# Kernel tuning notes

Hardware: AMD Instinct MI355X
Metric: run time of the kernel (lower is better)

Reference implementation:

```python
import jax, jax.numpy as jnp
import numpy as np

USER_NUM = 100000
ITEM_NUM = 100000  # padding index; table has ITEM_NUM+1 rows
D = 64
B = 4096
L = 200
NEG_WEIGHT = 0.1


def setup_inputs() -> dict:
    key = jax.random.key(0)
    k1, k2, k3, k4, k5 = jax.random.split(key, 5)
    uids = jax.random.randint(k1, (B,), 0, USER_NUM, dtype=jnp.int64 if jax.config.jax_enable_x64 else jnp.int32)
    pos_iids = jax.random.randint(k2, (B, L), 0, ITEM_NUM + 1, dtype=jnp.int64 if jax.config.jax_enable_x64 else jnp.int32)
    user_W = jax.random.normal(k3, (USER_NUM, D), dtype=jnp.float32) * 0.1
    item_W = jax.random.normal(k4, (ITEM_NUM + 1, D), dtype=jnp.float32) * 0.1
    h = jnp.full((D, 1), 0.01, dtype=jnp.float32)  # reset_para: constant 0.01
    return {"uids": uids, "pos_iids": pos_iids, "user_W": user_W, "item_W": item_W, "h": h}


def reference(uids, pos_iids, user_W, item_W, h):
    u_emb = user_W[uids]                      # [B, D] (dropout p=0 -> identity)
    pos_embs = item_W[pos_iids]               # [B, L, D]
    mask = (pos_iids != ITEM_NUM).astype(u_emb.dtype)  # padding id masked out
    pos_embs = pos_embs * mask[:, :, None]
    # hpq[b,l] = sum_d u[b,d] * pos[b,l,d] * h[d]
    hpq = jnp.einsum('bd,bld,d->bl', u_emb, pos_embs, h[:, 0])
    pos_data_loss = jnp.sum((1.0 - NEG_WEIGHT) * jnp.square(hpq) - 2.0 * hpq)
    # part_1/part_2 in torch are sums of per-row outer products == Gram matrices
    part_1 = item_W.T @ item_W                # [D, D]
    part_2 = u_emb.T @ u_emb                  # [D, D]
    part_3 = h @ h.T                          # [D, D]
    all_data_loss = jnp.sum(part_1 * part_2 * part_3)
    return NEG_WEIGHT * all_data_loss + pos_data_loss
```

## Files before the change

### kernel.cpp

```cpp
#include <hip/hip_runtime.h>

#define D 64
#define ITEM_PAD 100000
#define LSEQ 200
#define BATCH 4096
#define NEG_W 0.1f
#define NBI 512
#define NBU 64
#define GSZ (D * D)
#define PITEM_OFF 0
#define PUSER_OFF ((size_t)NBI * GSZ)
#define POS_OFF   (PUSER_OFF + (size_t)NBU * GSZ)
#define WS2_OFF   (POS_OFF + BATCH)
#define CTR_OFF   (WS2_OFF + 256)

__global__ void fused_partials(const int* __restrict__ uids,
                               const int* __restrict__ pos_iids,
                               const float* __restrict__ user_W,
                               const float* __restrict__ item_W,
                               const float* __restrict__ h,
                               float* __restrict__ ws) {
    __shared__ float smem[32 * D];
    const int bid = blockIdx.x;
    const int t   = threadIdx.x;

    if (bid == 0 && t == 0) ((unsigned*)(ws + CTR_OFF))[0] = 0u;

    if (bid < NBI + NBU) {
        const bool item = (bid < NBI);
        const float* __restrict__ W = item ? item_W : user_W;
        const int* __restrict__ idx = item ? nullptr : uids;
        const int nrows  = item ? (ITEM_PAD + 1) : BATCH;
        const int stride = item ? NBI : NBU;
        const int b0     = item ? bid : bid - NBI;
        float* __restrict__ out =
            ws + (item ? PITEM_OFF + (size_t)b0 * GSZ : PUSER_OFF + (size_t)b0 * GSZ);

        const int ti = t >> 4;
        const int tj = t & 15;
        float acc[4][4] = {{0.f,0.f,0.f,0.f},{0.f,0.f,0.f,0.f},
                           {0.f,0.f,0.f,0.f},{0.f,0.f,0.f,0.f}};

        const int nchunks = (nrows + 31) >> 5;

        float4 va = make_float4(0.f,0.f,0.f,0.f), vb = va;
        int c = b0;
        if (c < nchunks) {
            const int ra = (c << 5) + ti, rb = ra + 16;
            if (ra < nrows) {
                const int sa = idx ? idx[ra] : ra;
                va = *(const float4*)(W + (size_t)sa * D + tj * 4);
            }
            if (rb < nrows) {
                const int sb = idx ? idx[rb] : rb;
                vb = *(const float4*)(W + (size_t)sb * D + tj * 4);
            }
        }

        for (; c < nchunks; ) {
            __syncthreads();
            *(float4*)(smem + ti * D + tj * 4)        = va;
            *(float4*)(smem + (ti + 16) * D + tj * 4) = vb;
            __syncthreads();

            const int cn = c + stride;
            va = make_float4(0.f,0.f,0.f,0.f); vb = va;
            if (cn < nchunks) {
                const int ra = (cn << 5) + ti, rb = ra + 16;
                if (ra < nrows) {
                    const int sa = idx ? idx[ra] : ra;
                    va = *(const float4*)(W + (size_t)sa * D + tj * 4);
                }
                if (rb < nrows) {
                    const int sb = idx ? idx[rb] : rb;
                    vb = *(const float4*)(W + (size_t)sb * D + tj * 4);
                }
            }

            #pragma unroll
            for (int r2 = 0; r2 < 32; ++r2) {
                float xi[4], xj[4];
                *(float4*)xi = *(const float4*)(smem + r2 * D + ti * 4);
                *(float4*)xj = *(const float4*)(smem + r2 * D + tj * 4);
                #pragma unroll
                for (int a = 0; a < 4; ++a)
                    #pragma unroll
                    for (int b2 = 0; b2 < 4; ++b2)
                        acc[a][b2] += xi[a] * xj[b2];
            }
            c = cn;
        }
        #pragma unroll
        for (int a = 0; a < 4; ++a)
            *(float4*)(out + (ti * 4 + a) * D + tj * 4) = *(const float4*)acc[a];
    } else {
        const int b = bid - (NBI + NBU);
        float* uh   = smem;
        int*   sidx = (int*)(smem + D);
        float* red  = smem + D + LSEQ;

        if (t < LSEQ) sidx[t] = pos_iids[(size_t)b * LSEQ + t];
        if (t >= 192) {
            const int j = t - 192;
            uh[j] = user_W[(size_t)uids[b] * D + j] * h[j];
        }
        __syncthreads();

        const int lane = t & 63;
        const int wave = t >> 6;
        const int p    = lane >> 4;
        const int q    = lane & 15;
        const int base = wave * 4 + p;

        const float4 u4 = *(const float4*)(uh + q * 4);

        int ids[13];
        #pragma unroll
        for (int k = 0; k < 13; ++k) {
            const int l = base + 16 * k;
            ids[k] = (l < LSEQ) ? sidx[l] : ITEM_PAD;
        }
        float4 rows[13];
        #pragma unroll
        for (int k = 0; k < 13; ++k) {
            float4 v = make_float4(0.f, 0.f, 0.f, 0.f);
            if (ids[k] != ITEM_PAD)
                v = *(const float4*)(item_W + (size_t)ids[k] * D + q * 4);
            rows[k] = v;
        }

        float local = 0.f;
        #pragma unroll
        for (int k = 0; k < 13; ++k) {
            float s = u4.x*rows[k].x + u4.y*rows[k].y + u4.z*rows[k].z + u4.w*rows[k].w;
            s += __shfl_xor(s, 1);
            s += __shfl_xor(s, 2);
            s += __shfl_xor(s, 4);
            s += __shfl_xor(s, 8);
            if (q == 0)
                local += (1.0f - NEG_W) * s * s - 2.0f * s;
        }
        local += __shfl_xor(local, 1);
        local += __shfl_xor(local, 2);
        local += __shfl_xor(local, 4);
        local += __shfl_xor(local, 8);
        local += __shfl_xor(local, 16);
        local += __shfl_xor(local, 32);
        if (lane == 0) red[wave] = local;
        __syncthreads();
        if (t == 0)
            ws[POS_OFF + b] = red[0] + red[1] + red[2] + red[3];
    }
}

__global__ void reduce_final(const float* __restrict__ ws,
                             const float* __restrict__ h,
                             float* __restrict__ ws2,
                             unsigned* __restrict__ counter,
                             float* __restrict__ out) {
    __shared__ float rI[4][16];
    __shared__ float rU[4][16];
    __shared__ int isLast;
    const int b  = blockIdx.x;
    const int t  = threadIdx.x;
    const int kk = t & 15;
    const int ps = t >> 4;
    const int lane = t & 63;
    const int wave = t >> 6;
    const int k  = b * 16 + kk;

    float si = 0.f, su = 0.f;
    #pragma unroll 8
    for (int p = ps; p < NBI; p += 16) si += ws[PITEM_OFF + (size_t)p * GSZ + k];
    #pragma unroll
    for (int p = ps; p < NBU; p += 16) su += ws[PUSER_OFF + (size_t)p * GSZ + k];

    si += __shfl_xor(si, 16); si += __shfl_xor(si, 32);
    su += __shfl_xor(su, 16); su += __shfl_xor(su, 32);
    if (lane < 16) { rI[wave][kk] = si; rU[wave][kk] = su; }
    __syncthreads();

    float c = 0.f;
    if (t < 16) {
        const float Gi = rI[0][t] + rI[1][t] + rI[2][t] + rI[3][t];
        const float Gu = rU[0][t] + rU[1][t] + rU[2][t] + rU[3][t];
        const int kg = b * 16 + t;
        const int i = kg >> 6, j = kg & 63;
        c = NEG_W * Gi * Gu * h[i] * h[j] + ws[POS_OFF + b * 16 + t];
    }
    if (wave == 0) {
        c += __shfl_xor(c, 1);
        c += __shfl_xor(c, 2);
        c += __shfl_xor(c, 4);
        c += __shfl_xor(c, 8);
        if (lane == 0) ws2[b] = c;
    }

    if (t == 0) {
        __threadfence();
        const unsigned old = atomicAdd(counter, 1u);
        isLast = (old == 255u);
    }
    __syncthreads();
    if (isLast) {
        __threadfence();
        float s = ws2[t];
        s += __shfl_xor(s, 1);
        s += __shfl_xor(s, 2);
        s += __shfl_xor(s, 4);
        s += __shfl_xor(s, 8);
        s += __shfl_xor(s, 16);
        s += __shfl_xor(s, 32);
        __shared__ float red[4];
        if (lane == 0) red[wave] = s;
        __syncthreads();
        if (t == 0) out[0] = red[0] + red[1] + red[2] + red[3];
    }
}

extern "C" void kernel_launch(void* const* d_in, const int* in_sizes, int n_in,
                              void* d_out, int out_size, void* d_ws, size_t ws_size,
                              hipStream_t stream) {
    const int*   uids     = (const int*)d_in[0];
    const int*   pos_iids = (const int*)d_in[1];
    const float* user_W   = (const float*)d_in[2];
    const float* item_W   = (const float*)d_in[3];
    const float* h        = (const float*)d_in[4];
    float* out = (float*)d_out;
    float* ws  = (float*)d_ws;

    fused_partials<<<NBI + NBU + BATCH, 256, 0, stream>>>(uids, pos_iids, user_W,
                                                          item_W, h, ws);
    reduce_final<<<256, 256, 0, stream>>>(ws, h, ws + WS2_OFF,
                                          (unsigned*)(ws + CTR_OFF), out);
}
```

Before: 130.8 us.

## Convert item table to bf16 during Gram pass and gather bf16 rows for scores

```diff
diff --git a/kernel.cpp b/kernel.cpp
--- a/kernel.cpp
+++ b/kernel.cpp
@@ -8,45 +8,87 @@
 #define NBI 512
 #define NBU 64
 #define GSZ (D * D)
-#define PITEM_OFF 0
-#define PUSER_OFF ((size_t)NBI * GSZ)
-#define POS_OFF   (PUSER_OFF + (size_t)NBU * GSZ)
-#define WS2_OFF   (POS_OFF + BATCH)
-#define CTR_OFF   (WS2_OFF + 256)
-
-__global__ void fused_partials(const int* __restrict__ uids,
-                               const int* __restrict__ pos_iids,
-                               const float* __restrict__ user_W,
-                               const float* __restrict__ item_W,
-                               const float* __restrict__ h,
-                               float* __restrict__ ws) {
+
+#define BFT_FLOATS 3200032
+#define PITEM_OFF  ((size_t)BFT_FLOATS)
+#define PUSER_OFF  (PITEM_OFF + (size_t)NBI * GSZ)
+#define POS_OFF    (PUSER_OFF + (size_t)NBU * GSZ)
+#define GDOT_OFF   (POS_OFF + BATCH)
+
+__device__ __forceinline__ unsigned short f2bf_rne(float x) {
+    unsigned u = __builtin_bit_cast(unsigned, x);
+    return (unsigned short)((u + 0x7fffu + ((u >> 16) & 1u)) >> 16);
+}
+__device__ __forceinline__ float bf_lo(unsigned u) {
+    return __builtin_bit_cast(float, u << 16);
+}
+__device__ __forceinline__ float bf_hi(unsigned u) {
+    return __builtin_bit_cast(float, u & 0xffff0000u);
+}
+
+__global__ void gram_convert(const int* __restrict__ uids,
+                             const float* __restrict__ user_W,
+                             const float* __restrict__ item_W,
+                             float* __restrict__ ws) {
     __shared__ float smem[32 * D];
     const int bid = blockIdx.x;
     const int t   = threadIdx.x;
 
-    if (bid == 0 && t == 0) ((unsigned*)(ws + CTR_OFF))[0] = 0u;
-
-    if (bid < NBI + NBU) {
-        const bool item = (bid < NBI);
-        const float* __restrict__ W = item ? item_W : user_W;
-        const int* __restrict__ idx = item ? nullptr : uids;
-        const int nrows  = item ? (ITEM_PAD + 1) : BATCH;
-        const int stride = item ? NBI : NBU;
-        const int b0     = item ? bid : bid - NBI;
-        float* __restrict__ out =
-            ws + (item ? PITEM_OFF + (size_t)b0 * GSZ : PUSER_OFF + (size_t)b0 * GSZ);
-
-        const int ti = t >> 4;
-        const int tj = t & 15;
-        float acc[4][4] = {{0.f,0.f,0.f,0.f},{0.f,0.f,0.f,0.f},
-                           {0.f,0.f,0.f,0.f},{0.f,0.f,0.f,0.f}};
-
-        const int nchunks = (nrows + 31) >> 5;
-
-        float4 va = make_float4(0.f,0.f,0.f,0.f), vb = va;
-        int c = b0;
-        if (c < nchunks) {
+    const bool item = (bid < NBI);
+    const float* __restrict__ W = item ? item_W : user_W;
+    const int* __restrict__ idx = item ? nullptr : uids;
+    const int nrows  = item ? (ITEM_PAD + 1) : BATCH;
+    const int stride = item ? NBI : NBU;
+    const int b0     = item ? bid : bid - NBI;
+    float* __restrict__ out =
+        ws + (item ? PITEM_OFF + (size_t)b0 * GSZ : PUSER_OFF + (size_t)b0 * GSZ);
+    unsigned short* __restrict__ bft = (unsigned short*)ws;
+
+    const int ti = t >> 4;
+    const int tj = t & 15;
+    float acc[4][4] = {{0.f,0.f,0.f,0.f},{0.f,0.f,0.f,0.f},
+                       {0.f,0.f,0.f,0.f},{0.f,0.f,0.f,0.f}};
+
+    const int nchunks = (nrows + 31) >> 5;
+
+    float4 va = make_float4(0.f,0.f,0.f,0.f), vb = va;
+    int c = b0;
+    if (c < nchunks) {
+        const int ra = (c << 5) + ti, rb = ra + 16;
+        if (ra < nrows) {
+            const int sa = idx ? idx[ra] : ra;
+            va = *(const float4*)(W + (size_t)sa * D + tj * 4);
+        }
+        if (rb < nrows) {
+            const int sb = idx ? idx[rb] : rb;
+            vb = *(const float4*)(W + (size_t)sb * D + tj * 4);
+        }
+    }
+
+    while (c < nchunks) {
+        __syncthreads();
+        *(float4*)(smem + ti * D + tj * 4)        = va;
+        *(float4*)(smem + (ti + 16) * D + tj * 4) = vb;
+
+        if (item) {
             const int ra = (c << 5) + ti, rb = ra + 16;
+            if (ra < nrows) {
+                ushort4 s4 = { f2bf_rne(va.x), f2bf_rne(va.y),
+                               f2bf_rne(va.z), f2bf_rne(va.w) };
+                *(ushort4*)(bft + (size_t)ra * D + tj * 4) = s4;
+            }
+            if (rb < nrows) {
+                ushort4 s4 = { f2bf_rne(vb.x), f2bf_rne(vb.y),
+                               f2bf_rne(vb.z), f2bf_rne(vb.w) };
+                *(ushort4*)(bft + (size_t)rb * D + tj * 4) = s4;
+            }
+        }
+        __syncthreads();
+
+        const int cn = c + stride;
+        va = make_float4(0.f,0.f,0.f,0.f); vb = va;
+        if (cn < nchunks) {
+            const int ra = (cn << 5) + ti, rb = ra + 16;
             if (ra < nrows) {
                 const int sa = idx ? idx[ra] : ra;
                 va = *(const float4*)(W + (size_t)sa * D + tj * 4);
@@ -57,47 +99,40 @@
             }
         }
 
-        for (; c < nchunks; ) {
-            __syncthreads();
-            *(float4*)(smem + ti * D + tj * 4)        = va;
-            *(float4*)(smem + (ti + 16) * D + tj * 4) = vb;
-            __syncthreads();
-
-            const int cn = c + stride;
-            va = make_float4(0.f,0.f,0.f,0.f); vb = va;
-            if (cn < nchunks) {
-                const int ra = (cn << 5) + ti, rb = ra + 16;
-                if (ra < nrows) {
-                    const int sa = idx ? idx[ra] : ra;
-                    va = *(const float4*)(W + (size_t)sa * D + tj * 4);
-                }
-                if (rb < nrows) {
-                    const int sb = idx ? idx[rb] : rb;
-                    vb = *(const float4*)(W + (size_t)sb * D + tj * 4);
-                }
-            }
-
+        #pragma unroll
+        for (int r2 = 0; r2 < 32; ++r2) {
+            float xi[4], xj[4];
+            *(float4*)xi = *(const float4*)(smem + r2 * D + ti * 4);
+            *(float4*)xj = *(const float4*)(smem + r2 * D + tj * 4);
             #pragma unroll
-            for (int r2 = 0; r2 < 32; ++r2) {
-                float xi[4], xj[4];
-                *(float4*)xi = *(const float4*)(smem + r2 * D + ti * 4);
-                *(float4*)xj = *(const float4*)(smem + r2 * D + tj * 4);
+            for (int a = 0; a < 4; ++a)
                 #pragma unroll
-                for (int a = 0; a < 4; ++a)
-                    #pragma unroll
-                    for (int b2 = 0; b2 < 4; ++b2)
-                        acc[a][b2] += xi[a] * xj[b2];
-            }
-            c = cn;
-        }
-        #pragma unroll
-        for (int a = 0; a < 4; ++a)
-            *(float4*)(out + (ti * 4 + a) * D + tj * 4) = *(const float4*)acc[a];
-    } else {
-        const int b = bid - (NBI + NBU);
-        float* uh   = smem;
-        int*   sidx = (int*)(smem + D);
-        float* red  = smem + D + LSEQ;
+                for (int b2 = 0; b2 < 4; ++b2)
+                    acc[a][b2] += xi[a] * xj[b2];
+        }
+        c = cn;
+    }
+    #pragma unroll
+    for (int a = 0; a < 4; ++a)
+        *(float4*)(out + (ti * 4 + a) * D + tj * 4) = *(const float4*)acc[a];
+}
+
+__global__ void pos_and_reduce(const int* __restrict__ uids,
+                               const int* __restrict__ pos_iids,
+                               const float* __restrict__ user_W,
+                               const float* __restrict__ h,
+                               float* __restrict__ ws) {
+    const int bid = blockIdx.x;
+    const int t   = threadIdx.x;
+    const int lane = t & 63;
+    const int wave = t >> 6;
+
+    if (bid < BATCH) {
+        __shared__ float uh[D];
+        __shared__ int   sidx[LSEQ];
+        __shared__ float red[4];
+        const int b = bid;
+        const unsigned short* __restrict__ bft = (const unsigned short*)ws;
 
         if (t < LSEQ) sidx[t] = pos_iids[(size_t)b * LSEQ + t];
         if (t >= 192) {
@@ -106,37 +141,40 @@
         }
         __syncthreads();
 
-        const int lane = t & 63;
-        const int wave = t >> 6;
-        const int p    = lane >> 4;
-        const int q    = lane & 15;
-        const int base = wave * 4 + p;
-
-        const float4 u4 = *(const float4*)(uh + q * 4);
-
-        int ids[13];
-        #pragma unroll
-        for (int k = 0; k < 13; ++k) {
-            const int l = base + 16 * k;
+        const int p    = lane >> 3;
+        const int q    = lane & 7;
+        const int base = wave * 8 + p;
+
+        float u8[8];
+        *(float4*)(u8 + 0) = *(const float4*)(uh + q * 8);
+        *(float4*)(u8 + 4) = *(const float4*)(uh + q * 8 + 4);
+
+        int ids[7];
+        #pragma unroll
+        for (int k = 0; k < 7; ++k) {
+            const int l = base + 32 * k;
             ids[k] = (l < LSEQ) ? sidx[l] : ITEM_PAD;
         }
-        float4 rows[13];
-        #pragma unroll
-        for (int k = 0; k < 13; ++k) {
-            float4 v = make_float4(0.f, 0.f, 0.f, 0.f);
+        uint4 rows[7];
+        #pragma unroll
+        for (int k = 0; k < 7; ++k) {
+            uint4 v = make_uint4(0u, 0u, 0u, 0u);
             if (ids[k] != ITEM_PAD)
-                v = *(const float4*)(item_W + (size_t)ids[k] * D + q * 4);
+                v = *(const uint4*)(bft + (size_t)ids[k] * D + q * 8);
             rows[k] = v;
         }
 
         float local = 0.f;
         #pragma unroll
-        for (int k = 0; k < 13; ++k) {
-            float s = u4.x*rows[k].x + u4.y*rows[k].y + u4.z*rows[k].z + u4.w*rows[k].w;
+        for (int k = 0; k < 7; ++k) {
+            const uint4 v = rows[k];
+            float s = bf_lo(v.x)*u8[0] + bf_hi(v.x)*u8[1]
+                    + bf_lo(v.y)*u8[2] + bf_hi(v.y)*u8[3]
+                    + bf_lo(v.z)*u8[4] + bf_hi(v.z)*u8[5]
+                    + bf_lo(v.w)*u8[6] + bf_hi(v.w)*u8[7];
             s += __shfl_xor(s, 1);
             s += __shfl_xor(s, 2);
             s += __shfl_xor(s, 4);
-            s += __shfl_xor(s, 8);
             if (q == 0)
                 local += (1.0f - NEG_W) * s * s - 2.0f * s;
         }
@@ -150,72 +188,60 @@
         __syncthreads();
         if (t == 0)
             ws[POS_OFF + b] = red[0] + red[1] + red[2] + red[3];
+    } else {
+        __shared__ float rI[4][16];
+        __shared__ float rU[4][16];
+        const int bb = bid - BATCH;
+        const int kk = t & 15;
+        const int ps = t >> 4;
+        const int k  = bb * 16 + kk;
+
+        float si = 0.f, su = 0.f;
+        #pragma unroll 8
+        for (int p = ps; p < NBI; p += 16) si += ws[PITEM_OFF + (size_t)p * GSZ + k];
+        #pragma unroll
+        for (int p = ps; p < NBU; p += 16) su += ws[PUSER_OFF + (size_t)p * GSZ + k];
+
+        si += __shfl_xor(si, 16); si += __shfl_xor(si, 32);
+        su += __shfl_xor(su, 16); su += __shfl_xor(su, 32);
+        if (lane < 16) { rI[wave][kk] = si; rU[wave][kk] = su; }
+        __syncthreads();
+
+        if (wave == 0) {
+            float c = 0.f;
+            if (t < 16) {
+                const float Gi = rI[0][t] + rI[1][t] + rI[2][t] + rI[3][t];
+                const float Gu = rU[0][t] + rU[1][t] + rU[2][t] + rU[3][t];
+                const int kg = bb * 16 + t;
+                const int i = kg >> 6, j = kg & 63;
+                c = NEG_W * Gi * Gu * h[i] * h[j];
+            }
+            c += __shfl_xor(c, 1);
+            c += __shfl_xor(c, 2);
+            c += __shfl_xor(c, 4);
+            c += __shfl_xor(c, 8);
+            if (lane == 0) ws[GDOT_OFF + bb] = c;
+        }
     }
 }
 
-__global__ void reduce_final(const float* __restrict__ ws,
-                             const float* __restrict__ h,
-                             float* __restrict__ ws2,
-                             unsigned* __restrict__ counter,
-                             float* __restrict__ out) {
-    __shared__ float rI[4][16];
-    __shared__ float rU[4][16];
-    __shared__ int isLast;
-    const int b  = blockIdx.x;
-    const int t  = threadIdx.x;
-    const int kk = t & 15;
-    const int ps = t >> 4;
-    const int lane = t & 63;
-    const int wave = t >> 6;
-    const int k  = b * 16 + kk;
-
-    float si = 0.f, su = 0.f;
-    #pragma unroll 8
-    for (int p = ps; p < NBI; p += 16) si += ws[PITEM_OFF + (size_t)p * GSZ + k];
+__global__ void final_sum(const float* __restrict__ ws, float* __restrict__ out) {
+    __shared__ float red[4];
+    const int t = threadIdx.x;
+    float s = 0.f;
     #pragma unroll
-    for (int p = ps; p < NBU; p += 16) su += ws[PUSER_OFF + (size_t)p * GSZ + k];
-
-    si += __shfl_xor(si, 16); si += __shfl_xor(si, 32);
-    su += __shfl_xor(su, 16); su += __shfl_xor(su, 32);
-    if (lane < 16) { rI[wave][kk] = si; rU[wave][kk] = su; }
+    for (int k = 0; k < 17; ++k)
+        s += ws[POS_OFF + t + k * 256];
+    s += __shfl_xor(s, 1);
+    s += __shfl_xor(s, 2);
+    s += __shfl_xor(s, 4);
+    s += __shfl_xor(s, 8);
+    s += __shfl_xor(s, 16);
+    s += __shfl_xor(s, 32);
+    const int lane = t & 63, wave = t >> 6;
+    if (lane == 0) red[wave] = s;
     __syncthreads();
-
-    float c = 0.f;
-    if (t < 16) {
-        const float Gi = rI[0][t] + rI[1][t] + rI[2][t] + rI[3][t];
-        const float Gu = rU[0][t] + rU[1][t] + rU[2][t] + rU[3][t];
-        const int kg = b * 16 + t;
-        const int i = kg >> 6, j = kg & 63;
-        c = NEG_W * Gi * Gu * h[i] * h[j] + ws[POS_OFF + b * 16 + t];
-    }
-    if (wave == 0) {
-        c += __shfl_xor(c, 1);
-        c += __shfl_xor(c, 2);
-        c += __shfl_xor(c, 4);
-        c += __shfl_xor(c, 8);
-        if (lane == 0) ws2[b] = c;
-    }
-
-    if (t == 0) {
-        __threadfence();
-        const unsigned old = atomicAdd(counter, 1u);
-        isLast = (old == 255u);
-    }
-    __syncthreads();
-    if (isLast) {
-        __threadfence();
-        float s = ws2[t];
-        s += __shfl_xor(s, 1);
-        s += __shfl_xor(s, 2);
-        s += __shfl_xor(s, 4);
-        s += __shfl_xor(s, 8);
-        s += __shfl_xor(s, 16);
-        s += __shfl_xor(s, 32);
-        __shared__ float red[4];
-        if (lane == 0) red[wave] = s;
-        __syncthreads();
-        if (t == 0) out[0] = red[0] + red[1] + red[2] + red[3];
-    }
+    if (t == 0) out[0] = red[0] + red[1] + red[2] + red[3];
 }
 
 extern "C" void kernel_launch(void* const* d_in, const int* in_sizes, int n_in,
@@ -229,8 +255,7 @@
     float* out = (float*)d_out;
     float* ws  = (float*)d_ws;
 
-    fused_partials<<<NBI + NBU + BATCH, 256, 0, stream>>>(uids, pos_iids, user_W,
-                                                          item_W, h, ws);
-    reduce_final<<<256, 256, 0, stream>>>(ws, h, ws + WS2_OFF,
-                                          (unsigned*)(ws + CTR_OFF), out);
-}
+    gram_convert<<<NBI + NBU, 256, 0, stream>>>(uids, user_W, item_W, ws);
+    pos_and_reduce<<<BATCH + 256, 256, 0, stream>>>(uids, pos_iids, user_W, h, ws);
+    final_sum<<<1, 256, 0, stream>>>(ws, out);
+}
```

Result: faster. 122.9 us (-6.0%).

## Compute Gram partials with bf16 MFMA via transposed shared-memory tiles

Applied to the files above, without the earlier changes.

```diff
diff --git a/kernel.cpp b/kernel.cpp
--- a/kernel.cpp
+++ b/kernel.cpp
@@ -2,102 +2,116 @@
 
 #define D 64
 #define ITEM_PAD 100000
+#define NROWS_I (ITEM_PAD + 1)
 #define LSEQ 200
 #define BATCH 4096
 #define NEG_W 0.1f
 #define NBI 512
 #define NBU 64
 #define GSZ (D * D)
+#define TSTRIDE 40
+
 #define PITEM_OFF 0
 #define PUSER_OFF ((size_t)NBI * GSZ)
 #define POS_OFF   (PUSER_OFF + (size_t)NBU * GSZ)
-#define WS2_OFF   (POS_OFF + BATCH)
-#define CTR_OFF   (WS2_OFF + 256)
-
-__global__ void fused_partials(const int* __restrict__ uids,
-                               const int* __restrict__ pos_iids,
-                               const float* __restrict__ user_W,
-                               const float* __restrict__ item_W,
-                               const float* __restrict__ h,
-                               float* __restrict__ ws) {
-    __shared__ float smem[32 * D];
-    const int bid = blockIdx.x;
-    const int t   = threadIdx.x;
+#define WS3_OFF   (POS_OFF + BATCH)
+#define CTR_OFF   (WS3_OFF + 256)
+
+typedef __attribute__((ext_vector_type(8))) short short8;
+typedef __attribute__((ext_vector_type(4))) float f32x4;
+
+__device__ __forceinline__ unsigned short f2bf_rne(float x) {
+    unsigned u = __builtin_bit_cast(unsigned, x);
+    return (unsigned short)((u + 0x7fffu + ((u >> 16) & 1u)) >> 16);
+}
+
+__global__ void fused_all(const int* __restrict__ uids,
+                          const int* __restrict__ pos_iids,
+                          const float* __restrict__ user_W,
+                          const float* __restrict__ item_W,
+                          const float* __restrict__ h,
+                          float* __restrict__ ws) {
+    __shared__ unsigned short WtS[64 * TSTRIDE];
+    const int bid  = blockIdx.x;
+    const int t    = threadIdx.x;
+    const int lane = t & 63;
+    const int wave = t >> 6;
 
     if (bid == 0 && t == 0) ((unsigned*)(ws + CTR_OFF))[0] = 0u;
 
     if (bid < NBI + NBU) {
         const bool item = (bid < NBI);
         const float* __restrict__ W = item ? item_W : user_W;
-        const int* __restrict__ idx = item ? nullptr : uids;
-        const int nrows  = item ? (ITEM_PAD + 1) : BATCH;
+        const int nrows  = item ? NROWS_I : BATCH;
         const int stride = item ? NBI : NBU;
         const int b0     = item ? bid : bid - NBI;
         float* __restrict__ out =
             ws + (item ? PITEM_OFF + (size_t)b0 * GSZ : PUSER_OFF + (size_t)b0 * GSZ);
 
-        const int ti = t >> 4;
-        const int tj = t & 15;
-        float acc[4][4] = {{0.f,0.f,0.f,0.f},{0.f,0.f,0.f,0.f},
-                           {0.f,0.f,0.f,0.f},{0.f,0.f,0.f,0.f}};
+        const int rloc = t & 31;
+        const int c0   = (t >> 5) * 8;
+        const int m    = lane & 15;
+        const int g    = lane >> 4;
+
+        f32x4 acc[4] = {{0.f,0.f,0.f,0.f},{0.f,0.f,0.f,0.f},
+                        {0.f,0.f,0.f,0.f},{0.f,0.f,0.f,0.f}};
 
         const int nchunks = (nrows + 31) >> 5;
 
-        float4 va = make_float4(0.f,0.f,0.f,0.f), vb = va;
+        float4 pa = make_float4(0.f,0.f,0.f,0.f), pb = pa;
         int c = b0;
         if (c < nchunks) {
-            const int ra = (c << 5) + ti, rb = ra + 16;
-            if (ra < nrows) {
-                const int sa = idx ? idx[ra] : ra;
-                va = *(const float4*)(W + (size_t)sa * D + tj * 4);
+            const int r = (c << 5) + rloc;
+            if (r < nrows) {
+                const int src = item ? r : uids[r];
+                pa = *(const float4*)(W + (size_t)src * D + c0);
+                pb = *(const float4*)(W + (size_t)src * D + c0 + 4);
             }
-            if (rb < nrows) {
-                const int sb = idx ? idx[rb] : rb;
-                vb = *(const float4*)(W + (size_t)sb * D + tj * 4);
-            }
-        }
-
-        for (; c < nchunks; ) {
+        }
+
+        while (c < nchunks) {
+            unsigned short hb[8];
+            hb[0]=f2bf_rne(pa.x); hb[1]=f2bf_rne(pa.y); hb[2]=f2bf_rne(pa.z); hb[3]=f2bf_rne(pa.w);
+            hb[4]=f2bf_rne(pb.x); hb[5]=f2bf_rne(pb.y); hb[6]=f2bf_rne(pb.z); hb[7]=f2bf_rne(pb.w);
+
             __syncthreads();
-            *(float4*)(smem + ti * D + tj * 4)        = va;
-            *(float4*)(smem + (ti + 16) * D + tj * 4) = vb;
+            #pragma unroll
+            for (int j = 0; j < 8; ++j)
+                WtS[(c0 + j) * TSTRIDE + rloc] = hb[j];
             __syncthreads();
 
             const int cn = c + stride;
-            va = make_float4(0.f,0.f,0.f,0.f); vb = va;
+            pa = make_float4(0.f,0.f,0.f,0.f); pb = pa;
             if (cn < nchunks) {
-                const int ra = (cn << 5) + ti, rb = ra + 16;
-                if (ra < nrows) {
-                    const int sa = idx ? idx[ra] : ra;
-                    va = *(const float4*)(W + (size_t)sa * D + tj * 4);
-                }
-                if (rb < nrows) {
-                    const int sb = idx ? idx[rb] : rb;
-                    vb = *(const float4*)(W + (size_t)sb * D + tj * 4);
+                const int r = (cn << 5) + rloc;
+                if (r < nrows) {
+                    const int src = item ? r : uids[r];
+                    pa = *(const float4*)(W + (size_t)src * D + c0);
+                    pb = *(const float4*)(W + (size_t)src * D + c0 + 4);
                 }
             }
 
-            #pragma unroll
-            for (int r2 = 0; r2 < 32; ++r2) {
-                float xi[4], xj[4];
-                *(float4*)xi = *(const float4*)(smem + r2 * D + ti * 4);
-                *(float4*)xj = *(const float4*)(smem + r2 * D + tj * 4);
-                #pragma unroll
-                for (int a = 0; a < 4; ++a)
-                    #pragma unroll
-                    for (int b2 = 0; b2 < 4; ++b2)
-                        acc[a][b2] += xi[a] * xj[b2];
-            }
+            short8 frag[4];
+            #pragma unroll
+            for (int q = 0; q < 4; ++q)
+                frag[q] = *(const short8*)(&WtS[(q * 16 + m) * TSTRIDE + g * 8]);
+            #pragma unroll
+            for (int q = 0; q < 4; ++q)
+                acc[q] = __builtin_amdgcn_mfma_f32_16x16x32_bf16(frag[wave], frag[q],
+                                                                 acc[q], 0, 0, 0);
             c = cn;
         }
-        #pragma unroll
-        for (int a = 0; a < 4; ++a)
-            *(float4*)(out + (ti * 4 + a) * D + tj * 4) = *(const float4*)acc[a];
+
+        #pragma unroll
+        for (int q = 0; q < 4; ++q)
+            #pragma unroll
+            for (int reg = 0; reg < 4; ++reg)
+                out[(wave * 16 + g * 4 + reg) * D + q * 16 + m] = acc[q][reg];
     } else {
         const int b = bid - (NBI + NBU);
-        float* uh   = smem;
-        int*   sidx = (int*)(smem + D);
-        float* red  = smem + D + LSEQ;
+        float* uh   = (float*)WtS;
+        int*   sidx = (int*)WtS + 64;
+        float* red  = (float*)WtS + 264;
 
         if (t < LSEQ) sidx[t] = pos_iids[(size_t)b * LSEQ + t];
         if (t >= 192) {
@@ -106,8 +120,6 @@
         }
         __syncthreads();
 
-        const int lane = t & 63;
-        const int wave = t >> 6;
         const int p    = lane >> 4;
         const int q    = lane & 15;
         const int base = wave * 4 + p;
@@ -155,19 +167,19 @@
 
 __global__ void reduce_final(const float* __restrict__ ws,
                              const float* __restrict__ h,
-                             float* __restrict__ ws2,
+                             float* __restrict__ ws3,
                              unsigned* __restrict__ counter,
                              float* __restrict__ out) {
     __shared__ float rI[4][16];
     __shared__ float rU[4][16];
     __shared__ int isLast;
-    const int b  = blockIdx.x;
+    const int bb = blockIdx.x;
     const int t  = threadIdx.x;
     const int kk = t & 15;
     const int ps = t >> 4;
     const int lane = t & 63;
     const int wave = t >> 6;
-    const int k  = b * 16 + kk;
+    const int k  = bb * 16 + kk;
 
     float si = 0.f, su = 0.f;
     #pragma unroll 8
@@ -180,31 +192,30 @@
     if (lane < 16) { rI[wave][kk] = si; rU[wave][kk] = su; }
     __syncthreads();
 
-    float c = 0.f;
-    if (t < 16) {
-        const float Gi = rI[0][t] + rI[1][t] + rI[2][t] + rI[3][t];
-        const float Gu = rU[0][t] + rU[1][t] + rU[2][t] + rU[3][t];
-        const int kg = b * 16 + t;
-        const int i = kg >> 6, j = kg & 63;
-        c = NEG_W * Gi * Gu * h[i] * h[j] + ws[POS_OFF + b * 16 + t];
-    }
     if (wave == 0) {
+        float c = 0.f;
+        if (t < 16) {
+            const float Gi = rI[0][t] + rI[1][t] + rI[2][t] + rI[3][t];
+            const float Gu = rU[0][t] + rU[1][t] + rU[2][t] + rU[3][t];
+            const int kg = bb * 16 + t;
+            const int i = kg >> 6, j = kg & 63;
+            c = NEG_W * Gi * Gu * h[i] * h[j] + ws[POS_OFF + bb * 16 + t];
+        }
         c += __shfl_xor(c, 1);
         c += __shfl_xor(c, 2);
         c += __shfl_xor(c, 4);
         c += __shfl_xor(c, 8);
-        if (lane == 0) ws2[b] = c;
+        if (lane == 0) ws3[bb] = c;
     }
 
     if (t == 0) {
         __threadfence();
-        const unsigned old = atomicAdd(counter, 1u);
-        isLast = (old == 255u);
+        isLast = (atomicAdd(counter, 1u) == 255u);
     }
     __syncthreads();
     if (isLast) {
         __threadfence();
-        float s = ws2[t];
+        float s = ws3[t];
         s += __shfl_xor(s, 1);
         s += __shfl_xor(s, 2);
         s += __shfl_xor(s, 4);
@@ -229,8 +240,8 @@
     float* out = (float*)d_out;
     float* ws  = (float*)d_ws;
 
-    fused_partials<<<NBI + NBU + BATCH, 256, 0, stream>>>(uids, pos_iids, user_W,
-                                                          item_W, h, ws);
-    reduce_final<<<256, 256, 0, stream>>>(ws, h, ws + WS2_OFF,
+    fused_all<<<NBI + NBU + BATCH, 256, 0, stream>>>(uids, pos_iids, user_W,
+                                                     item_W, h, ws);
+    reduce_final<<<256, 256, 0, stream>>>(ws, h, ws + WS3_OFF,
                                           (unsigned*)(ws + CTR_OFF), out);
 }
```

Result: slower. 133.9 us (+2.4%).
